# Optimization experiments

Measured on AMD Instinct MI355X. Metric: run time of the kernel, lower is better.

The kernel has to match this reference:

```python
import jax, jax.numpy as jnp
import numpy as np

C = 1000      # num_classes
U = 10        # proxies_per_class
D = 512       # feature_dim
B = 4096      # batch
ALPHA = 32.0
DELTA = 0.1


def _l2norm(x, axis=-1):
    return x / jnp.linalg.norm(x, axis=axis, keepdims=True).clip(1e-12)


def setup_inputs() -> dict:
    key = jax.random.key(0)
    k1, k2, k3 = jax.random.split(key, 3)
    features = jax.random.normal(k1, (B, D), dtype=jnp.float32)
    labels = jax.random.randint(k2, (B,), 0, C)
    # proxies are initialized to row-normalized gaussians (as in __init__)
    proxies = _l2norm(jax.random.normal(k3, (C * U, D), dtype=jnp.float32))
    return {"features": features, "labels": labels, "proxies": proxies}


def reference(features, labels, proxies):
    # proxy_class_ids: [C*U], class id of each proxy
    class_ids = jnp.repeat(jnp.arange(C), U)

    x = _l2norm(features)          # [B, D]
    p = _l2norm(proxies)           # [P, D], P = C*U
    sim = x @ p.T                  # [B, P]

    # ---- infer_logits, agg='soft', tau=1 ----
    s = sim.reshape(B, C, U)       # per-class proxy similarities
    w = jax.nn.softmax(s, axis=2)
    logits = jnp.sum(w * s, axis=2)  # [B, C], tau=1 so no extra scaling

    # ---- _compute_proxy_loss (Proxy-Anchor) ----
    sim_t = sim.T                                         # [P, B]
    pos_mask = labels[None, :] == class_ids[:, None]      # [P, B]
    neg_inf = jnp.finfo(jnp.float32).min
    z_pos = jnp.where(pos_mask, -ALPHA * (sim_t - DELTA), neg_inf)
    z_neg = jnp.where(pos_mask, neg_inf, ALPHA * (sim_t + DELTA))
    lse_pos = jax.nn.logsumexp(z_pos, axis=1)             # [P]
    lse_neg = jax.nn.logsumexp(z_neg, axis=1)             # [P]
    pos_term = jax.nn.softplus(lse_pos)
    neg_term = jax.nn.softplus(lse_neg)
    has_pos = pos_mask.any(axis=1)
    pos_loss = jnp.where(has_pos, pos_term, 0.0).sum() / jnp.maximum(
        has_pos.sum(), 1).astype(jnp.float32)
    neg_loss = neg_term.mean()
    proxy_loss = pos_loss + neg_loss

    return logits, proxy_loss
```

## Files before the change

### kernel.cpp

```cpp
#include <hip/hip_runtime.h>
#include <hip/hip_bf16.h>

#define C_CLS   1000
#define U_PX    10
#define D_DIM   512
#define B_BATCH 4096
#define P_PX    (C_CLS * U_PX)
#define ALPHA_F 32.0f
#define DELTA_F 0.1f

#define BM 256
#define BN 80
#define BK 64
#define SIMP 84
#define NKS (D_DIM / BK)

#define A_OFF    0
#define B_OFF    32768
#define B_STRIDE 10240
#define SMEM_SZ  (32768 + 2 * B_STRIDE)

#define ZERO_DBL (2 * P_PX + 4)
#define FIN_BLK  ((P_PX + 255) / 256)

typedef __attribute__((ext_vector_type(8))) short bf16x8;
typedef __attribute__((ext_vector_type(4))) float f32x4;

typedef __attribute__((address_space(1))) const void gv_t;
typedef __attribute__((address_space(3))) void lv_t;

__device__ __forceinline__ void gload_lds16(const void* g, void* lds) {
    __builtin_amdgcn_global_load_lds((gv_t*)g, (lv_t*)lds, 16, 0, 0);
}

__device__ __forceinline__ unsigned int f2bf(float f) {
    union { float f; unsigned u; } c; c.f = f;
    unsigned u = c.u;
    return (u + 0x7FFF + ((u >> 16) & 1)) >> 16;
}

__global__ __launch_bounds__(256) void norm_rows_kernel(const float* __restrict__ feat,
                                                        const float* __restrict__ prox,
                                                        unsigned int* __restrict__ xout,
                                                        unsigned int* __restrict__ pout,
                                                        double* __restrict__ zbase) {
    const int zidx = blockIdx.x * 256 + threadIdx.x;
    if (zidx < ZERO_DBL) zbase[zidx] = 0.0;

    const int wid  = threadIdx.x >> 6;
    const int lane = threadIdx.x & 63;
    int row = blockIdx.x * 4 + wid;
    const float* in;
    unsigned int* out;
    if (row < B_BATCH) { in = feat + (size_t)row * D_DIM;   out = xout + (size_t)row * (D_DIM / 2); }
    else { row -= B_BATCH; in = prox + (size_t)row * D_DIM; out = pout + (size_t)row * (D_DIM / 2); }
    const float4 v0 = reinterpret_cast<const float4*>(in)[lane * 2];
    const float4 v1 = reinterpret_cast<const float4*>(in)[lane * 2 + 1];
    float ss = v0.x*v0.x + v0.y*v0.y + v0.z*v0.z + v0.w*v0.w
             + v1.x*v1.x + v1.y*v1.y + v1.z*v1.z + v1.w*v1.w;
    #pragma unroll
    for (int off = 1; off < 64; off <<= 1) ss += __shfl_xor(ss, off, 64);
    const float inv = 1.0f / fmaxf(sqrtf(ss), 1e-12f);
    uint4 o;
    o.x = f2bf(v0.x * inv) | (f2bf(v0.y * inv) << 16);
    o.y = f2bf(v0.z * inv) | (f2bf(v0.w * inv) << 16);
    o.z = f2bf(v1.x * inv) | (f2bf(v1.y * inv) << 16);
    o.w = f2bf(v1.z * inv) | (f2bf(v1.w * inv) << 16);
    *reinterpret_cast<uint4*>(out + lane * 4) = o;
}

__global__ __launch_bounds__(256, 3) void fused_gemm_kernel(
    const unsigned short* __restrict__ xbf,
    const unsigned short* __restrict__ pbf,
    const int*            __restrict__ labels,
    float*                __restrict__ logits,
    double*               __restrict__ pos_sum,
    double*               __restrict__ neg_sum)
{
    __shared__ __align__(16) char smem[SMEM_SZ];
    __shared__ int lab_lds[BM];

    const int t    = threadIdx.x;
    const int m0   = blockIdx.x * BM;
    const int n0   = blockIdx.y * BN;
    const int wid  = t >> 6;
    const int lane = t & 63;
    const int l15  = lane & 15;
    const int kgrp = lane >> 4;

    if (t < BM) lab_lds[t] = labels[m0 + t];

    const int srow = lane >> 3;
    const int scol = (lane & 7) ^ srow;

    const int koff0 = ((kgrp    ) ^ (l15 & 7)) << 4;
    const int koff1 = ((kgrp + 4) ^ (l15 & 7)) << 4;

    f32x4 acc[4][5];
    #pragma unroll
    for (int m = 0; m < 4; ++m)
        #pragma unroll
        for (int n = 0; n < 5; ++n) acc[m][n] = (f32x4){0.f, 0.f, 0.f, 0.f};

    #define STAGE_A(ks_)                                                                \
        do {                                                                            \
            const int kb_ = (ks_) * BK;                                                 \
            _Pragma("unroll")                                                           \
            for (int i = 0; i < 8; ++i) {                                               \
                const int c_ = wid * 8 + i;                                             \
                gload_lds16(xbf + (size_t)(m0 + c_ * 8 + srow) * D_DIM + kb_ + scol * 8,\
                            smem + A_OFF + c_ * 1024);                                  \
            }                                                                           \
        } while (0)

    #define STAGE_B(ks_, buf_)                                                          \
        do {                                                                            \
            const int kb_ = (ks_) * BK;                                                 \
            char* bb_ = smem + B_OFF + (buf_) * B_STRIDE;                               \
            for (int c_ = wid; c_ < 10; c_ += 4)                                        \
                gload_lds16(pbf + (size_t)(n0 + c_ * 8 + srow) * D_DIM + kb_ + scol * 8,\
                            bb_ + c_ * 1024);                                           \
        } while (0)

    STAGE_B(0, 0);
    STAGE_A(0);
    asm volatile("s_waitcnt vmcnt(0)\n\ts_barrier" ::: "memory");

    for (int ks = 0; ks < NKS; ++ks) {
        const char* bbase = smem + B_OFF + (ks & 1) * B_STRIDE;
        if (ks < NKS - 1) STAGE_B(ks + 1, (ks + 1) & 1);
        __builtin_amdgcn_s_setprio(1);
        #pragma unroll
        for (int kk8 = 0; kk8 < 2; ++kk8) {
            const int koff = kk8 ? koff1 : koff0;
            bf16x8 b[5];
            #pragma unroll
            for (int n = 0; n < 5; ++n)
                b[n] = *reinterpret_cast<const bf16x8*>(bbase + (n * 16 + l15) * 128 + koff);
            #pragma unroll
            for (int m = 0; m < 4; ++m) {
                const bf16x8 a = *reinterpret_cast<const bf16x8*>(
                    smem + A_OFF + (wid * 64 + m * 16 + l15) * 128 + koff);
                #pragma unroll
                for (int n = 0; n < 5; ++n)
                    acc[m][n] = __builtin_amdgcn_mfma_f32_16x16x32_bf16(a, b[n], acc[m][n], 0, 0, 0);
            }
        }
        __builtin_amdgcn_s_setprio(0);
        asm volatile("s_waitcnt lgkmcnt(0)" ::: "memory");
        __builtin_amdgcn_sched_barrier(0);
        if (ks < NKS - 1) STAGE_A(ks + 1);
        asm volatile("s_waitcnt vmcnt(0)\n\ts_barrier" ::: "memory");
    }

    {
        int labv[16];
        #pragma unroll
        for (int m = 0; m < 4; ++m)
            #pragma unroll
            for (int r = 0; r < 4; ++r)
                labv[m * 4 + r] = lab_lds[wid * 64 + m * 16 + kgrp * 4 + r];
        #pragma unroll
        for (int n = 0; n < 5; ++n) {
            const int col = n * 16 + l15;
            const int cls = (n0 + col) / U_PX;
            float pos = 0.f, neg = 0.f;
            #pragma unroll
            for (int m = 0; m < 4; ++m)
                #pragma unroll
                for (int r = 0; r < 4; ++r) {
                    const float s = acc[m][n][r];
                    const bool isp = (labv[m * 4 + r] == cls);
                    const float e = __expf(isp ? (-ALPHA_F * (s - DELTA_F))
                                               : ( ALPHA_F * (s + DELTA_F)));
                    if (isp) pos += e; else neg += e;
                }
            pos += __shfl_xor(pos, 16, 64); pos += __shfl_xor(pos, 32, 64);
            neg += __shfl_xor(neg, 16, 64); neg += __shfl_xor(neg, 32, 64);
            if (lane < 16) {
                atomicAdd(&neg_sum[n0 + col], (double)neg);
                if (pos != 0.f) atomicAdd(&pos_sum[n0 + col], (double)pos);
            }
        }
    }

    float* simw = reinterpret_cast<float*>(smem) + wid * (16 * SIMP);
    #pragma unroll
    for (int m = 0; m < 4; ++m) {
        #pragma unroll
        for (int n = 0; n < 5; ++n)
            #pragma unroll
            for (int r = 0; r < 4; ++r)
                simw[(kgrp * 4 + r) * SIMP + n * 16 + l15] = acc[m][n][r];
        #pragma unroll
        for (int it = 0; it < 2; ++it) {
            const int j   = lane + it * 64;
            const int r   = j >> 3;
            const int c   = j & 7;
            const float* s = simw + r * SIMP + c * U_PX;
            float wsum = 0.f, wssum = 0.f;
            #pragma unroll
            for (int u = 0; u < U_PX; ++u) {
                const float sv = s[u];
                const float e = __expf(sv);
                wsum += e; wssum += e * sv;
            }
            logits[(size_t)(m0 + wid * 64 + m * 16 + r) * C_CLS + (n0 / U_PX + c)] = wssum / wsum;
        }
        __builtin_amdgcn_s_waitcnt(0);
    }
}

__global__ __launch_bounds__(256) void finalize_kernel(
    const double* __restrict__ pos_sum,
    const double* __restrict__ neg_sum,
    double*       __restrict__ accum,
    float*        __restrict__ out_loss)
{
    const int p = blockIdx.x * 256 + threadIdx.x;
    double pv = 0.0, nv = 0.0;
    int c = 0;
    if (p < P_PX) {
        nv = log1p(neg_sum[p]);
        const double ps = pos_sum[p];
        if (ps != 0.0) { pv = log1p(ps); c = 1; }
    }
    #pragma unroll
    for (int off = 1; off < 64; off <<= 1) {
        pv += __shfl_xor(pv, off, 64);
        nv += __shfl_xor(nv, off, 64);
        c  += __shfl_xor(c,  off, 64);
    }
    if ((threadIdx.x & 63) == 0) {
        atomicAdd(&accum[0], pv);
        atomicAdd(&accum[1], nv);
        atomicAdd((int*)(accum + 2), c);
    }
    __syncthreads();
    __threadfence();
    if (threadIdx.x == 0) {
        const unsigned prev = atomicAdd((unsigned*)(accum + 3), 1u);
        if (prev == FIN_BLK - 1) {
            const double a0 = atomicAdd(&accum[0], 0.0);
            const double a1 = atomicAdd(&accum[1], 0.0);
            const int   cnt = atomicAdd((int*)(accum + 2), 0);
            out_loss[0] = (float)(a0 / (double)max(cnt, 1) + a1 / (double)P_PX);
        }
    }
}

extern "C" void kernel_launch(void* const* d_in, const int* in_sizes, int n_in,
                              void* d_out, int out_size, void* d_ws, size_t ws_size,
                              hipStream_t stream) {
    const float* features = (const float*)d_in[0];
    const int*   labels   = (const int*)d_in[1];
    const float* proxies  = (const float*)d_in[2];
    float* out = (float*)d_out;

    char* ws = (char*)d_ws;
    unsigned short* xbf = (unsigned short*)ws;
    unsigned short* pbf = (unsigned short*)(ws + (size_t)B_BATCH * D_DIM * 2);
    double* pos_sum = (double*)(ws + (size_t)(B_BATCH + P_PX) * D_DIM * 2);
    double* neg_sum = pos_sum + P_PX;
    double* accum   = neg_sum + P_PX;

    norm_rows_kernel<<<(B_BATCH + P_PX) / 4, 256, 0, stream>>>(
        features, proxies, (unsigned int*)xbf, (unsigned int*)pbf, pos_sum);

    fused_gemm_kernel<<<dim3(B_BATCH / BM, P_PX / BN), 256, 0, stream>>>(
        xbf, pbf, labels, out, pos_sum, neg_sum);

    finalize_kernel<<<FIN_BLK, 256, 0, stream>>>(pos_sum, neg_sum, accum,
                                                 out + (size_t)B_BATCH * C_CLS);
}
```

Measured before the change: 97.40 us.

## Preload K-step fragments into registers and overlap next-tile global loads with MFMAs

Drops the double-buffered B tile in LDS. Each K step now reads all A and B fragments into registers, barriers, then issues the global-to-LDS loads for both A and B of the next step before running the MFMA chain. This lets the A-tile loads overlap compute instead of being issued after it, and it shrinks the LDS footprint, which could raise occupancy. In exchange it uses more registers to hold the fragments and adds an extra barrier per K step.

Result: slower. 149.4 us (+53.4%).

```diff
diff --git a/kernel.cpp b/kernel.cpp
--- a/kernel.cpp
+++ b/kernel.cpp
@@ -15,10 +15,9 @@
 #define SIMP 84
 #define NKS (D_DIM / BK)
 
-#define A_OFF    0
-#define B_OFF    32768
-#define B_STRIDE 10240
-#define SMEM_SZ  (32768 + 2 * B_STRIDE)
+#define A_OFF   0
+#define B_OFF   32768
+#define SMEM_SZ 43008
 
 #define ZERO_DBL (2 * P_PX + 4)
 #define FIN_BLK  ((P_PX + 255) / 256)
@@ -113,43 +112,47 @@
             }                                                                           \
         } while (0)
 
-    #define STAGE_B(ks_, buf_)                                                          \
+    #define STAGE_B(ks_)                                                                \
         do {                                                                            \
             const int kb_ = (ks_) * BK;                                                 \
-            char* bb_ = smem + B_OFF + (buf_) * B_STRIDE;                               \
             for (int c_ = wid; c_ < 10; c_ += 4)                                        \
                 gload_lds16(pbf + (size_t)(n0 + c_ * 8 + srow) * D_DIM + kb_ + scol * 8,\
-                            bb_ + c_ * 1024);                                           \
+                            smem + B_OFF + c_ * 1024);                                  \
         } while (0)
 
-    STAGE_B(0, 0);
     STAGE_A(0);
+    STAGE_B(0);
     asm volatile("s_waitcnt vmcnt(0)\n\ts_barrier" ::: "memory");
 
     for (int ks = 0; ks < NKS; ++ks) {
-        const char* bbase = smem + B_OFF + (ks & 1) * B_STRIDE;
-        if (ks < NKS - 1) STAGE_B(ks + 1, (ks + 1) & 1);
+        bf16x8 aF[4][2], bF[5][2];
+        #pragma unroll
+        for (int k8 = 0; k8 < 2; ++k8) {
+            const int koff = k8 ? koff1 : koff0;
+            #pragma unroll
+            for (int n = 0; n < 5; ++n)
+                bF[n][k8] = *reinterpret_cast<const bf16x8*>(
+                    smem + B_OFF + (n * 16 + l15) * 128 + koff);
+            #pragma unroll
+            for (int m = 0; m < 4; ++m)
+                aF[m][k8] = *reinterpret_cast<const bf16x8*>(
+                    smem + A_OFF + (wid * 64 + m * 16 + l15) * 128 + koff);
+        }
+        asm volatile("s_waitcnt lgkmcnt(0)" ::: "memory");
+        __builtin_amdgcn_sched_barrier(0);
+        __builtin_amdgcn_s_barrier();
+        if (ks < NKS - 1) { STAGE_A(ks + 1); STAGE_B(ks + 1); }
         __builtin_amdgcn_s_setprio(1);
         #pragma unroll
-        for (int kk8 = 0; kk8 < 2; ++kk8) {
-            const int koff = kk8 ? koff1 : koff0;
-            bf16x8 b[5];
-            #pragma unroll
-            for (int n = 0; n < 5; ++n)
-                b[n] = *reinterpret_cast<const bf16x8*>(bbase + (n * 16 + l15) * 128 + koff);
-            #pragma unroll
-            for (int m = 0; m < 4; ++m) {
-                const bf16x8 a = *reinterpret_cast<const bf16x8*>(
-                    smem + A_OFF + (wid * 64 + m * 16 + l15) * 128 + koff);
+        for (int k8 = 0; k8 < 2; ++k8)
+            #pragma unroll
+            for (int m = 0; m < 4; ++m)
                 #pragma unroll
                 for (int n = 0; n < 5; ++n)
-                    acc[m][n] = __builtin_amdgcn_mfma_f32_16x16x32_bf16(a, b[n], acc[m][n], 0, 0, 0);
-            }
-        }
+                    acc[m][n] = __builtin_amdgcn_mfma_f32_16x16x32_bf16(
+                        aF[m][k8], bF[n][k8], acc[m][n], 0, 0, 0);
         __builtin_amdgcn_s_setprio(0);
-        asm volatile("s_waitcnt lgkmcnt(0)" ::: "memory");
         __builtin_amdgcn_sched_barrier(0);
-        if (ks < NKS - 1) STAGE_A(ks + 1);
         asm volatile("s_waitcnt vmcnt(0)\n\ts_barrier" ::: "memory");
     }
 
```
